# Kernel optimization log

Hardware: AMD Instinct MI355X
Metric: run time of the kernel (lower is better)

## Reference

```python
import jax, jax.numpy as jnp
import numpy as np

D_MODEL = 1024
N_HEADS = 16


def setup_inputs() -> dict:
    key = jax.random.key(0)
    ks = jax.random.split(key, 7)
    scale = 1.0 / np.sqrt(D_MODEL)
    seq = jax.random.normal(ks[0], (4, 1024, D_MODEL), dtype=jnp.float32)
    Wq = jax.random.normal(ks[1], (D_MODEL, D_MODEL), dtype=jnp.float32) * scale
    bq = jax.random.normal(ks[2], (D_MODEL,), dtype=jnp.float32) * 0.02
    Wk = jax.random.normal(ks[3], (D_MODEL, D_MODEL), dtype=jnp.float32) * scale
    bk = jax.random.normal(ks[4], (D_MODEL,), dtype=jnp.float32) * 0.02
    Wv = jax.random.normal(ks[5], (D_MODEL, D_MODEL), dtype=jnp.float32) * scale
    bv = jax.random.normal(ks[6], (D_MODEL,), dtype=jnp.float32) * 0.02
    return {"seq": seq, "Wq": Wq, "bq": bq, "Wk": Wk, "bk": bk, "Wv": Wv, "bv": bv}


def reference(seq, Wq, bq, Wk, bk, Wv, bv):
    B, S, D = seq.shape
    H = N_HEADS
    dv = D // H
    # nn.Linear: x @ W.T + b; W stored [out, in]
    q = (seq @ Wq.T + bq).reshape(B, S, H, dv).transpose(0, 2, 1, 3)  # [B,H,S,dv]
    k = (seq @ Wk.T + bk).reshape(B, S, H, dv).transpose(0, 2, 1, 3)
    v = (seq @ Wv.T + bv).reshape(B, S, H, dv).transpose(0, 2, 1, 3)
    scores = jnp.einsum('bhqd,bhkd->bhqk', q, k) / jnp.sqrt(jnp.asarray(dv, seq.dtype))
    p = jax.nn.softmax(scores, axis=-1)
    out = jnp.einsum('bhqk,bhkd->bhqd', p, v)  # [B,H,S,dv]
    return out.transpose(0, 2, 1, 3).reshape(B, S, D)
```

## Files before the change

### kernel.cpp

```cpp
#include <hip/hip_runtime.h>
#include <hip/hip_fp16.h>

typedef _Float16 f16x8 __attribute__((ext_vector_type(8)));
typedef _Float16 f16x4 __attribute__((ext_vector_type(4)));
typedef float f32x4 __attribute__((ext_vector_type(4)));
typedef float f32x16 __attribute__((ext_vector_type(16)));

#define D_MODEL 1024
#define SEQ 1024
#define BATCH 4
#define NH 16
#define DV 64
#define M_TOTAL (BATCH * SEQ)
#define QBLK 128

__device__ __forceinline__ void gload16(const _Float16* g, _Float16* lds) {
    __builtin_amdgcn_global_load_lds((const __attribute__((address_space(1))) void*)g,
                                     (__attribute__((address_space(3))) void*)lds,
                                     16, 0, 0);
}

__global__ void cvt_f32_f16(const float* __restrict__ s, _Float16* __restrict__ d, int n) {
    int i = (blockIdx.x * blockDim.x + threadIdx.x) * 8;
    if (i >= n) return;
    float4 a = *(const float4*)(s + i);
    float4 b = *(const float4*)(s + i + 4);
    f16x8 h;
    h[0] = (_Float16)a.x; h[1] = (_Float16)a.y; h[2] = (_Float16)a.z; h[3] = (_Float16)a.w;
    h[4] = (_Float16)b.x; h[5] = (_Float16)b.y; h[6] = (_Float16)b.z; h[7] = (_Float16)b.w;
    *(f16x8*)(d + i) = h;
}

__global__ void cvt3_f32_f16(const float* __restrict__ s0, const float* __restrict__ s1,
                             const float* __restrict__ s2, _Float16* __restrict__ d0,
                             _Float16* __restrict__ d1, _Float16* __restrict__ d2, int n) {
    const float* s = (blockIdx.y == 0) ? s0 : (blockIdx.y == 1 ? s1 : s2);
    _Float16*    d = (blockIdx.y == 0) ? d0 : (blockIdx.y == 1 ? d1 : d2);
    int i = (blockIdx.x * blockDim.x + threadIdx.x) * 8;
    if (i >= n) return;
    float4 a = *(const float4*)(s + i);
    float4 b = *(const float4*)(s + i + 4);
    f16x8 h;
    h[0] = (_Float16)a.x; h[1] = (_Float16)a.y; h[2] = (_Float16)a.z; h[3] = (_Float16)a.w;
    h[4] = (_Float16)b.x; h[5] = (_Float16)b.y; h[6] = (_Float16)b.z; h[7] = (_Float16)b.w;
    *(f16x8*)(d + i) = h;
}

__global__ __launch_bounds__(512, 2) void qkv_gemm(
    const _Float16* __restrict__ X,
    const _Float16* __restrict__ W0, const _Float16* __restrict__ W1, const _Float16* __restrict__ W2,
    const float* __restrict__ b0, const float* __restrict__ b1, const float* __restrict__ b2,
    _Float16* __restrict__ Qo, _Float16* __restrict__ Ko, _Float16* __restrict__ Vto)
{
    __shared__ _Float16 SM[4 * 256 * 64];
#define ABASE(buf) (SM + (buf) * 16384)
#define BBASE(buf) (SM + 32768 + (buf) * 16384)

    const int tid = threadIdx.x;
    const int l = tid & 63;
    const int w = tid >> 6;
    const int wr = w >> 2, wc = w & 3;

    const int bid = blockIdx.x;
    const int nid = (bid & 7) * 24 + (bid >> 3);
    const int mt = nid & 15, ntg = nid >> 4;
    const int mat = ntg >> 2, nt = ntg & 3;
    const _Float16* Wm  = (mat == 0) ? W0 : (mat == 1 ? W1 : W2);
    const float*    bia = (mat == 0) ? b0 : (mat == 1 ? b1 : b2);
    const int m0 = mt * 256, n0 = nt * 256;

    const int str = tid >> 3;
    const int sc8 = ((tid & 7) ^ (str & 7)) * 8;
    const _Float16* xsrc = X  + (size_t)(m0 + str) * D_MODEL + sc8;
    const _Float16* wsrc = Wm + (size_t)(n0 + str) * D_MODEL + sc8;
    const int ldst = str * 64 + (tid & 7) * 8;

#define SA(buf, kt, h) do { \
    gload16(xsrc + (size_t)((h) * 128) * D_MODEL + (kt) * 64, ABASE(buf) + (h) * 8192 + ldst); \
    gload16(xsrc + (size_t)((h) * 128 + 64) * D_MODEL + (kt) * 64, ABASE(buf) + (h) * 8192 + 4096 + ldst); } while (0)
#define SB(buf, kt, h) do { \
    gload16(wsrc + (size_t)((h) * 128) * D_MODEL + (kt) * 64, BBASE(buf) + (h) * 8192 + ldst); \
    gload16(wsrc + (size_t)((h) * 128 + 64) * D_MODEL + (kt) * 64, BBASE(buf) + (h) * 8192 + 4096 + ldst); } while (0)

    const int fr = l & 15, g = l >> 4, fr7 = l & 7;
    const int wrow = wr * 128, bcol = wc * 64;

    f32x4 acc[8][4] = {};
    f16x8 b[4][2];

    SB(0, 0, 0); SB(0, 0, 1);
    SA(0, 0, 0); SA(0, 0, 1);
    SB(1, 1, 0); SB(1, 1, 1);
    asm volatile("s_waitcnt vmcnt(4)" ::: "memory");
    __builtin_amdgcn_s_barrier();

#define PHASES(BUF, TSA_BUF, TSA, TSB_BUF, TSB)                                              \
    _Pragma("unroll")                                                                        \
    for (int p = 0; p < 4; ++p) {                                                            \
        if (p == 0) {                                                                        \
            _Pragma("unroll")                                                                \
            for (int nj = 0; nj < 4; ++nj) {                                                 \
                const int rb = (bcol + nj * 16 + fr) * 64;                                   \
                b[nj][0] = *(const f16x8*)&BBASE(BUF)[rb + ((g ^ fr7) << 3)];                \
                b[nj][1] = *(const f16x8*)&BBASE(BUF)[rb + (((4 + g) ^ fr7) << 3)];          \
            }                                                                                \
        }                                                                                    \
        f16x8 aq[2][2];                                                                      \
        _Pragma("unroll")                                                                    \
        for (int q = 0; q < 2; ++q) {                                                        \
            const int ra = (wrow + (2 * p + q) * 16 + fr) * 64;                              \
            aq[q][0] = *(const f16x8*)&ABASE(BUF)[ra + ((g ^ fr7) << 3)];                    \
            aq[q][1] = *(const f16x8*)&ABASE(BUF)[ra + (((4 + g) ^ fr7) << 3)];              \
        }                                                                                    \
        if (p == 0) SA(TSA_BUF, TSA, 0);                                                     \
        else if (p == 1) SA(TSA_BUF, TSA, 1);                                                \
        else if (p == 2) SB(TSB_BUF, TSB, 0);                                                \
        else SB(TSB_BUF, TSB, 1);                                                            \
        __builtin_amdgcn_s_barrier();                                                        \
        __builtin_amdgcn_s_setprio(1);                                                       \
        _Pragma("unroll")                                                                    \
        for (int ks = 0; ks < 2; ++ks)                                                       \
            _Pragma("unroll")                                                                \
            for (int q = 0; q < 2; ++q)                                                      \
                _Pragma("unroll")                                                            \
                for (int nj = 0; nj < 4; ++nj)                                               \
                    acc[2 * p + q][nj] = __builtin_amdgcn_mfma_f32_16x16x32_f16(             \
                        aq[q][ks], b[nj][ks], acc[2 * p + q][nj], 0, 0, 0);                  \
        __builtin_amdgcn_s_setprio(0);                                                       \
        if (p == 3) asm volatile("s_waitcnt vmcnt(4)" ::: "memory");                         \
        __builtin_amdgcn_s_barrier();                                                        \
    }

    for (int it = 0; it < 8; ++it) {
        const int tA = 2 * it + 1;
        const int tN = (2 * it + 2 < 16) ? 2 * it + 2 : 15;
        const int tM = (2 * it + 3 < 16) ? 2 * it + 3 : 15;
        PHASES(0, 1, tA, 0, tN)
        PHASES(1, 0, tN, 1, tM)
    }
#undef PHASES
#undef SA
#undef SB

    if (mat != 2) {
        const float scale = (mat == 0) ? 0.125f * 1.44269504088896340736f : 1.0f;
#pragma unroll
        for (int nj = 0; nj < 4; ++nj) {
            const int o = n0 + bcol + nj * 16 + fr;
            const float bb = bia[o];
            const int h = o >> 6, dd = o & 63;
#pragma unroll
            for (int mi = 0; mi < 8; ++mi) {
#pragma unroll
                for (int r = 0; r < 4; ++r) {
                    const int m = m0 + wrow + mi * 16 + g * 4 + r;
                    const int bi = m >> 10, s = m & 1023;
                    const float v = (acc[mi][nj][r] + bb) * scale;
                    const _Float16 hv = (_Float16)v;
                    const int bh = bi * NH + h;
                    if (mat == 0) Qo[((size_t)bh * SEQ + s) * DV + dd] = hv;
                    else          Ko[((size_t)bh * SEQ + s) * DV + dd] = hv;
                }
            }
        }
    } else {
        asm volatile("s_waitcnt vmcnt(0)" ::: "memory");
        __syncthreads();
#pragma unroll
        for (int nj = 0; nj < 4; ++nj) {
            const int n = bcol + nj * 16 + fr;
            const float bb = bia[n0 + n];
#pragma unroll
            for (int mi = 0; mi < 8; ++mi) {
#pragma unroll
                for (int r = 0; r < 4; ++r) {
                    const int m = wrow + mi * 16 + g * 4 + r;
                    SM[n * 256 + ((((m >> 3) + n) & 31) << 3) + (m & 7)] =
                        (_Float16)(acc[mi][nj][r] + bb);
                }
            }
        }
        __syncthreads();
        const int bi = m0 >> 10, s0 = m0 & 1023;
#pragma unroll
        for (int itp = 0; itp < 16; ++itp) {
            const int task = itp * 512 + tid;
            const int dd = task >> 5, sc = task & 31;
            f16x8 vv = *(const f16x8*)&SM[dd * 256 + (((sc + dd) & 31) << 3)];
            const int og = n0 + dd;
            const int h = og >> 6, d = og & 63;
            const int bh = bi * NH + h;
            *(f16x8*)(Vto + ((size_t)bh * DV + d) * SEQ + s0 + sc * 8) = vv;
        }
    }
#undef ABASE
#undef BBASE
}

__global__ __launch_bounds__(512, 4) void attn(
    const _Float16* __restrict__ Q, const _Float16* __restrict__ K,
    const _Float16* __restrict__ Vt, float* __restrict__ out)
{
    __shared__ _Float16 Kb[4][64 * 64];
    __shared__ _Float16 Vb[4][64 * 64];

    const int tid = threadIdx.x;
    const int w = tid >> 6, l = tid & 63;
    const int grp = w >> 2, wl = w & 3;
    const int q_ = l & 31, hl = l >> 5;

    const int fid = blockIdx.y * 8 + blockIdx.x;
    const int nid = (fid & 7) * 64 + (fid >> 3);
    const int bh = nid >> 3, qt = nid & 7;
    const int b = bh >> 4, h = bh & 15;
    const int q0 = qt * QBLK + wl * 32;

    const int half = tid >> 8;
    const int gt = tid & 255;
    const int str = gt >> 3;
    const int scs = ((gt & 7) ^ (str & 7)) * 8;
    const int ldst = str * 64 + (gt & 7) * 8;
    const _Float16* Kg = K  + (size_t)bh * SEQ * DV;
    const _Float16* Vg = Vt + (size_t)bh * DV * SEQ;

    f16x8 qf[4];
    {
        const _Float16* qp = Q + ((size_t)bh * SEQ + q0 + q_) * DV + hl * 8;
#pragma unroll
        for (int c = 0; c < 4; ++c) qf[c] = *(const f16x8*)(qp + c * 16);
    }

    float m_run = -1e30f, l_run = 0.f;
    f32x16 acc0 = {}, acc1 = {};

#define STAGET(T) do {                                                                    \
        const int slot = (T) & 3;                                                         \
        gload16(Kg + (size_t)((T) * 64 + str) * DV + scs, &Kb[slot][0] + ldst);           \
        gload16(Kg + (size_t)((T) * 64 + str + 32) * DV + scs, &Kb[slot][32 * 64] + ldst);\
        gload16(Vg + (size_t)str * SEQ + (T) * 64 + scs, &Vb[slot][0] + ldst);            \
        gload16(Vg + (size_t)(str + 32) * SEQ + (T) * 64 + scs, &Vb[slot][32 * 64] + ldst);\
    } while (0)

#define QK(S, slot, kt) do {                                                              \
        S = (f32x16){};                                                                   \
        const int row = (kt) * 32 + q_;                                                   \
        _Pragma("unroll")                                                                 \
        for (int c = 0; c < 4; ++c) {                                                     \
            f16x8 kf = *(const f16x8*)&Kb[slot][row * 64 + (((c * 2 + hl) ^ (row & 7)) << 3)]; \
            S = __builtin_amdgcn_mfma_f32_32x32x16_f16(kf, qf[c], S, 0, 0, 0);            \
        }                                                                                 \
    } while (0)

#define SMPV(S, slot, kt) do {                                                            \
        float lmax = S[0];                                                                \
        _Pragma("unroll")                                                                 \
        for (int r = 1; r < 16; ++r) lmax = fmaxf(lmax, S[r]);                            \
        const float mm = fmaxf(lmax, __shfl_xor(lmax, 32));                               \
        if (!__all(mm - m_run <= 8.0f)) {                                                 \
            const float mn = fmaxf(m_run, mm);                                            \
            const float al = exp2f(m_run - mn);                                           \
            l_run *= al;                                                                  \
            acc0 *= al; acc1 *= al;                                                       \
            m_run = mn;                                                                   \
        }                                                                                 \
        float p[16];                                                                      \
        float rsum = 0.f;                                                                 \
        _Pragma("unroll")                                                                 \
        for (int r = 0; r < 16; ++r) { p[r] = exp2f(S[r] - m_run); rsum += p[r]; }        \
        l_run += rsum;                                                                    \
        f16x4 pf[4];                                                                      \
        _Pragma("unroll")                                                                 \
        for (int G = 0; G < 4; ++G) {                                                     \
            pf[G][0] = (_Float16)p[4 * G];     pf[G][1] = (_Float16)p[4 * G + 1];         \
            pf[G][2] = (_Float16)p[4 * G + 2]; pf[G][3] = (_Float16)p[4 * G + 3];         \
        }                                                                                 \
        __builtin_amdgcn_s_setprio(1);                                                    \
        _Pragma("unroll")                                                                 \
        for (int G = 0; G < 4; ++G) {                                                     \
            const int c16 = (kt) * 4 + G;                                                 \
            const int r0 = q_;                                                            \
            f16x4 v0 = *(const f16x4*)&Vb[slot][r0 * 64 + (((c16) ^ (r0 & 7)) << 3) + hl * 4]; \
            acc0 = __builtin_amdgcn_mfma_f32_32x32x8f16(v0, pf[G], acc0, 0, 0, 0);        \
            const int r1 = 32 + q_;                                                       \
            f16x4 v1 = *(const f16x4*)&Vb[slot][r1 * 64 + (((c16) ^ (r1 & 7)) << 3) + hl * 4]; \
            acc1 = __builtin_amdgcn_mfma_f32_32x32x8f16(v1, pf[G], acc1, 0, 0, 0);        \
        }                                                                                 \
        __builtin_amdgcn_s_setprio(0);                                                    \
    } while (0)

    STAGET(half);
    __syncthreads();

    for (int i = 0; i < 8; ++i) {
        const int T = 2 * i + grp;
        const int slot = T & 3;
        if (i < 7) STAGET(2 * i + 2 + half);

        f32x16 s0, s1;
        QK(s0, slot, 0);
        QK(s1, slot, 1);
        SMPV(s0, slot, 0);
        SMPV(s1, slot, 1);

        __syncthreads();
    }
#undef STAGET
#undef QK
#undef SMPV

    l_run += __shfl_xor(l_run, 32);

    float* Ob = (float*)&Kb[0][0];
    float* Ml = (float*)&Vb[0][0];
    if (grp == 1) {
        float* dst = Ob + (wl * 64 + l) * 32;
#pragma unroll
        for (int r = 0; r < 16; ++r) { dst[r] = acc0[r]; dst[16 + r] = acc1[r]; }
        if (l < 32) {
            Ml[(wl * 32 + q_) * 2]     = m_run;
            Ml[(wl * 32 + q_) * 2 + 1] = l_run;
        }
    }
    __syncthreads();
    if (grp == 0) {
        const float m1 = Ml[(wl * 32 + q_) * 2];
        const float l1 = Ml[(wl * 32 + q_) * 2 + 1];
        const float M  = fmaxf(m_run, m1);
        const float e0 = exp2f(m_run - M);
        const float e1 = exp2f(m1 - M);
        const float inv = 1.0f / (e0 * l_run + e1 * l1);
        const float* src = Ob + (wl * 64 + l) * 32;
        float* ob = out + ((size_t)b * SEQ + q0 + q_) * D_MODEL + h * DV;
#pragma unroll
        for (int rg = 0; rg < 4; ++rg) {
            float4 v4;
            const int d0 = rg * 8 + 4 * hl;
            v4.x = (acc0[4 * rg + 0] * e0 + src[4 * rg + 0] * e1) * inv;
            v4.y = (acc0[4 * rg + 1] * e0 + src[4 * rg + 1] * e1) * inv;
            v4.z = (acc0[4 * rg + 2] * e0 + src[4 * rg + 2] * e1) * inv;
            v4.w = (acc0[4 * rg + 3] * e0 + src[4 * rg + 3] * e1) * inv;
            *(float4*)(ob + d0) = v4;
            v4.x = (acc1[4 * rg + 0] * e0 + src[16 + 4 * rg + 0] * e1) * inv;
            v4.y = (acc1[4 * rg + 1] * e0 + src[16 + 4 * rg + 1] * e1) * inv;
            v4.z = (acc1[4 * rg + 2] * e0 + src[16 + 4 * rg + 2] * e1) * inv;
            v4.w = (acc1[4 * rg + 3] * e0 + src[16 + 4 * rg + 3] * e1) * inv;
            *(float4*)(ob + 32 + d0) = v4;
        }
    }
}

extern "C" void kernel_launch(void* const* d_in, const int* in_sizes, int n_in,
                              void* d_out, int out_size, void* d_ws, size_t ws_size,
                              hipStream_t stream) {
    const float* seq = (const float*)d_in[0];
    const float* Wq  = (const float*)d_in[1];
    const float* bq  = (const float*)d_in[2];
    const float* Wk  = (const float*)d_in[3];
    const float* bk  = (const float*)d_in[4];
    const float* Wv  = (const float*)d_in[5];
    const float* bv  = (const float*)d_in[6];
    float* out = (float*)d_out;

    _Float16* seqh = (_Float16*)d_ws;
    _Float16* wqh  = seqh + (size_t)M_TOTAL * D_MODEL;
    _Float16* wkh  = wqh + (size_t)D_MODEL * D_MODEL;
    _Float16* wvh  = wkh + (size_t)D_MODEL * D_MODEL;
    _Float16* Qh   = wvh + (size_t)D_MODEL * D_MODEL;
    _Float16* Kh   = Qh + (size_t)M_TOTAL * D_MODEL;
    _Float16* Vth  = Kh + (size_t)M_TOTAL * D_MODEL;

    const int n_seq = M_TOTAL * D_MODEL;
    const int n_w   = D_MODEL * D_MODEL;
    cvt_f32_f16<<<n_seq / (256 * 8), 256, 0, stream>>>(seq, seqh, n_seq);
    cvt3_f32_f16<<<dim3(n_w / (256 * 8), 3), 256, 0, stream>>>(Wq, Wk, Wv, wqh, wkh, wvh, n_w);

    qkv_gemm<<<192, 512, 0, stream>>>(
        seqh, wqh, wkh, wvh, bq, bk, bv, Qh, Kh, Vth);

    attn<<<dim3(SEQ / QBLK, BATCH * NH), 512, 0, stream>>>(Qh, Kh, Vth, out);
}
```

Baseline: 81.87 us.

## Use 32x32x16 MFMA for PV with cross-half P shuffle and tree reductions

Replaces the eight 32x32x8 MFMAs per tile in the P·V step with four 32x32x16 MFMAs. The P fragments are repacked across the two 32-lane halves with xor-32 shuffles so each lane holds eight consecutive keys, and V is read as 16-byte LDS loads. The row max and sum become tree reductions, the fp16 conversion uses packed cvt_pkrtz, and the attention loop is fully unrolled. This cuts MFMA issue count and LDS instructions per tile, at the cost of extra shuffles and more register pressure from the unroll. cvt_pkrtz rounds toward zero, which slightly changes how P is rounded.

```diff
diff --git a/kernel.cpp b/kernel.cpp
--- a/kernel.cpp
+++ b/kernel.cpp
@@ -18,6 +18,13 @@
     __builtin_amdgcn_global_load_lds((const __attribute__((address_space(1))) void*)g,
                                      (__attribute__((address_space(3))) void*)lds,
                                      16, 0, 0);
+}
+
+__device__ __forceinline__ unsigned pk16(float a, float b) {
+    auto h = __builtin_amdgcn_cvt_pkrtz(a, b);
+    unsigned r;
+    __builtin_memcpy(&r, &h, 4);
+    return r;
 }
 
 __global__ void cvt_f32_f16(const float* __restrict__ s, _Float16* __restrict__ d, int n) {
@@ -234,11 +241,11 @@
     f32x16 acc0 = {}, acc1 = {};
 
 #define STAGET(T) do {                                                                    \
-        const int slot = (T) & 3;                                                         \
-        gload16(Kg + (size_t)((T) * 64 + str) * DV + scs, &Kb[slot][0] + ldst);           \
-        gload16(Kg + (size_t)((T) * 64 + str + 32) * DV + scs, &Kb[slot][32 * 64] + ldst);\
-        gload16(Vg + (size_t)str * SEQ + (T) * 64 + scs, &Vb[slot][0] + ldst);            \
-        gload16(Vg + (size_t)(str + 32) * SEQ + (T) * 64 + scs, &Vb[slot][32 * 64] + ldst);\
+        const int slot_ = (T) & 3;                                                        \
+        gload16(Kg + (size_t)((T) * 64 + str) * DV + scs, &Kb[slot_][0] + ldst);          \
+        gload16(Kg + (size_t)((T) * 64 + str + 32) * DV + scs, &Kb[slot_][32 * 64] + ldst);\
+        gload16(Vg + (size_t)str * SEQ + (T) * 64 + scs, &Vb[slot_][0] + ldst);           \
+        gload16(Vg + (size_t)(str + 32) * SEQ + (T) * 64 + scs, &Vb[slot_][32 * 64] + ldst);\
     } while (0)
 
 #define QK(S, slot, kt) do {                                                              \
@@ -252,9 +259,12 @@
     } while (0)
 
 #define SMPV(S, slot, kt) do {                                                            \
-        float lmax = S[0];                                                                \
-        _Pragma("unroll")                                                                 \
-        for (int r = 1; r < 16; ++r) lmax = fmaxf(lmax, S[r]);                            \
+        float mx8[8];                                                                     \
+        _Pragma("unroll")                                                                 \
+        for (int j = 0; j < 8; ++j) mx8[j] = fmaxf(S[j], S[j + 8]);                       \
+        float mx4a = fmaxf(mx8[0], mx8[4]), mx4b = fmaxf(mx8[1], mx8[5]);                 \
+        float mx4c = fmaxf(mx8[2], mx8[6]), mx4d = fmaxf(mx8[3], mx8[7]);                 \
+        const float lmax = fmaxf(fmaxf(mx4a, mx4b), fmaxf(mx4c, mx4d));                   \
         const float mm = fmaxf(lmax, __shfl_xor(lmax, 32));                               \
         if (!__all(mm - m_run <= 8.0f)) {                                                 \
             const float mn = fmaxf(m_run, mm);                                            \
@@ -264,26 +274,43 @@
             m_run = mn;                                                                   \
         }                                                                                 \
         float p[16];                                                                      \
-        float rsum = 0.f;                                                                 \
-        _Pragma("unroll")                                                                 \
-        for (int r = 0; r < 16; ++r) { p[r] = exp2f(S[r] - m_run); rsum += p[r]; }        \
-        l_run += rsum;                                                                    \
-        f16x4 pf[4];                                                                      \
+        _Pragma("unroll")                                                                 \
+        for (int r = 0; r < 16; ++r) p[r] = exp2f(S[r] - m_run);                          \
+        float rs8[8];                                                                     \
+        _Pragma("unroll")                                                                 \
+        for (int j = 0; j < 8; ++j) rs8[j] = p[j] + p[j + 8];                             \
+        float rs4a = rs8[0] + rs8[4], rs4b = rs8[1] + rs8[5];                             \
+        float rs4c = rs8[2] + rs8[6], rs4d = rs8[3] + rs8[7];                             \
+        l_run += (rs4a + rs4b) + (rs4c + rs4d);                                           \
+        unsigned u[4][2];                                                                 \
         _Pragma("unroll")                                                                 \
         for (int G = 0; G < 4; ++G) {                                                     \
-            pf[G][0] = (_Float16)p[4 * G];     pf[G][1] = (_Float16)p[4 * G + 1];         \
-            pf[G][2] = (_Float16)p[4 * G + 2]; pf[G][3] = (_Float16)p[4 * G + 3];         \
+            u[G][0] = pk16(p[4 * G], p[4 * G + 1]);                                       \
+            u[G][1] = pk16(p[4 * G + 2], p[4 * G + 3]);                                   \
         }                                                                                 \
         __builtin_amdgcn_s_setprio(1);                                                    \
         _Pragma("unroll")                                                                 \
-        for (int G = 0; G < 4; ++G) {                                                     \
-            const int c16 = (kt) * 4 + G;                                                 \
+        for (int wv = 0; wv < 2; ++wv) {                                                  \
+            const unsigned a00 = u[2 * wv][0], a01 = u[2 * wv][1];                        \
+            const unsigned a10 = u[2 * wv + 1][0], a11 = u[2 * wv + 1][1];                \
+            const unsigned s00 = (unsigned)__shfl_xor((int)a00, 32);                      \
+            const unsigned s01 = (unsigned)__shfl_xor((int)a01, 32);                      \
+            const unsigned s10 = (unsigned)__shfl_xor((int)a10, 32);                      \
+            const unsigned s11 = (unsigned)__shfl_xor((int)a11, 32);                      \
+            unsigned wd[4];                                                               \
+            wd[0] = hl ? s10 : a00;                                                       \
+            wd[1] = hl ? s11 : a01;                                                       \
+            wd[2] = hl ? a10 : s00;                                                       \
+            wd[3] = hl ? a11 : s01;                                                       \
+            f16x8 pb;                                                                     \
+            __builtin_memcpy(&pb, wd, 16);                                                \
+            const int c16 = (kt) * 4 + 2 * wv + hl;                                       \
             const int r0 = q_;                                                            \
-            f16x4 v0 = *(const f16x4*)&Vb[slot][r0 * 64 + (((c16) ^ (r0 & 7)) << 3) + hl * 4]; \
-            acc0 = __builtin_amdgcn_mfma_f32_32x32x8f16(v0, pf[G], acc0, 0, 0, 0);        \
+            f16x8 v0 = *(const f16x8*)&Vb[slot][r0 * 64 + (((c16) ^ (r0 & 7)) << 3)];     \
+            acc0 = __builtin_amdgcn_mfma_f32_32x32x16_f16(v0, pb, acc0, 0, 0, 0);         \
             const int r1 = 32 + q_;                                                       \
-            f16x4 v1 = *(const f16x4*)&Vb[slot][r1 * 64 + (((c16) ^ (r1 & 7)) << 3) + hl * 4]; \
-            acc1 = __builtin_amdgcn_mfma_f32_32x32x8f16(v1, pf[G], acc1, 0, 0, 0);        \
+            f16x8 v1 = *(const f16x8*)&Vb[slot][r1 * 64 + (((c16) ^ (r1 & 7)) << 3)];     \
+            acc1 = __builtin_amdgcn_mfma_f32_32x32x16_f16(v1, pb, acc1, 0, 0, 0);         \
         }                                                                                 \
         __builtin_amdgcn_s_setprio(0);                                                    \
     } while (0)
@@ -291,6 +318,7 @@
     STAGET(half);
     __syncthreads();
 
+#pragma unroll
     for (int i = 0; i < 8; ++i) {
         const int T = 2 * i + grp;
         const int slot = T & 3;
```

Measured after the change: 84.60 us. 1.03x slower.
